# Kernel tuning notes

Measured on AMD Instinct MI355X. Metric: run time of the kernel, lower is better.

Reference implementation:

```python
import jax, jax.numpy as jnp
import numpy as np

B, S, D, H = 4, 2048, 1024, 16
DK = D // H


def setup_inputs() -> dict:
    key = jax.random.key(0)
    ks = jax.random.split(key, 12)
    def lin(k):
        # torch nn.Linear default init scale ~ 1/sqrt(fan_in); use small normal
        return jax.random.normal(k, (D, D), dtype=jnp.float32) * (1.0 / np.sqrt(D))
    inp = {
        "query": jax.random.normal(ks[0], (B, S, D), dtype=jnp.float32),
        "key":   jax.random.normal(ks[1], (B, S, D), dtype=jnp.float32),
        "value": jax.random.normal(ks[2], (B, S, D), dtype=jnp.float32),
        "Wq": lin(ks[3]), "bq": jax.random.normal(ks[4], (D,), dtype=jnp.float32) * 0.01,
        "Wk": lin(ks[5]), "bk": jax.random.normal(ks[6], (D,), dtype=jnp.float32) * 0.01,
        "Wv": lin(ks[7]), "bv": jax.random.normal(ks[8], (D,), dtype=jnp.float32) * 0.01,
        "Wo": lin(ks[9]), "bo": jax.random.normal(ks[10], (D,), dtype=jnp.float32) * 0.01,
        # causal mask, True = attend (masked_fill where mask == 0)
        "causal_mask": jnp.tril(jnp.ones((S, S), dtype=bool))[None, None, :, :],
    }
    return inp


def reference(query, key, value, Wq, bq, Wk, bk, Wv, bv, Wo, bo, causal_mask):
    # Linear projections (torch Linear: y = x @ W.T + b), split heads -> [B,H,S,DK]
    def proj(x, W, b):
        return (x @ W.T + b).reshape(B, S, H, DK).transpose(0, 2, 1, 3)
    Q = proj(query, Wq, bq)
    K = proj(key, Wk, bk)
    V = proj(value, Wv, bv)
    scale = 1.0 / jnp.sqrt(jnp.float32(DK))
    scores = jnp.einsum('bhqd,bhkd->bhqk', Q, K) * scale  # [B,H,S,S]
    scores = jnp.where(causal_mask, scores, -jnp.inf)
    attn = jax.nn.softmax(scores, axis=-1)
    out = jnp.einsum('bhqk,bhkd->bhqd', attn, V)  # [B,H,S,DK]
    out = out.transpose(0, 2, 1, 3).reshape(B, S, D)
    return out @ Wo.T + bo
```

## Files before the change

kernel.cpp:

```cpp
#include <hip/hip_runtime.h>
#include <stdint.h>

#define SLEN   2048
#define DMODEL 1024
#define NHEAD  16
#define DKH    64
#define BATCH  4

typedef unsigned short ushort_t;
typedef __bf16         bf16x8 __attribute__((ext_vector_type(8)));
typedef unsigned short u16x8  __attribute__((ext_vector_type(8)));
typedef unsigned short u16x4  __attribute__((ext_vector_type(4)));
typedef unsigned int   u32x4  __attribute__((ext_vector_type(4)));
typedef float          f32x4  __attribute__((ext_vector_type(4)));

#define QSCALE 0.18033688f

__device__ __forceinline__ ushort_t f2bf(float f) {
  unsigned int u = __builtin_bit_cast(unsigned int, f);
  u += 0x7fffu + ((u >> 16) & 1u);
  return (ushort_t)(u >> 16);
}
__device__ __forceinline__ unsigned pk2(float a, float b) {
  const unsigned ua = __builtin_bit_cast(unsigned, a) + 0x8000u;
  const unsigned ub = __builtin_bit_cast(unsigned, b) + 0x8000u;
  return __builtin_amdgcn_perm(ub, ua, 0x07060302u);
}
__device__ __forceinline__ u16x8 cvt8f(const float* p) {
  f32x4 a = *(const f32x4*)p;
  f32x4 b = *(const f32x4*)(p + 4);
  u32x4 w;
  w[0] = pk2(a[0], a[1]);
  w[1] = pk2(a[2], a[3]);
  w[2] = pk2(b[0], b[1]);
  w[3] = pk2(b[2], b[3]);
  return __builtin_bit_cast(u16x8, w);
}

typedef __attribute__((address_space(1))) void gvoid_t;
typedef __attribute__((address_space(3))) void lvoid_t;
__device__ __forceinline__ void gld_lds16(const void* g, void* l) {
  __builtin_amdgcn_global_load_lds((gvoid_t*)(g), (lvoid_t*)(l), 16, 0, 0);
}

__device__ __forceinline__ int swz(int row, int c) {
  return row * 64 + (c ^ ((row & 7) * 8));
}
__device__ __forceinline__ int sx4(int r) { return (r ^ (r >> 2)) & 3; }

__global__ __launch_bounds__(256) void cvt_all(
    const float* __restrict__ Wq, const float* __restrict__ Wk,
    const float* __restrict__ Wv, const float* __restrict__ Wo,
    const float* __restrict__ q, const float* __restrict__ k,
    const float* __restrict__ v,
    ushort_t* __restrict__ Wbf, ushort_t* __restrict__ Xq,
    ushort_t* __restrict__ Xk,  ushort_t* __restrict__ Xv) {
  const int b = blockIdx.x;
  if (b < 2048) {
    const int gid = b * 256 + threadIdx.x;
    const int seg = gid >> 17;
    const int off = (gid & 131071) * 8;
    const float* src = (seg == 0) ? Wq : (seg == 1) ? Wk : (seg == 2) ? Wv : Wo;
    *(u16x8*)&Wbf[((size_t)seg << 20) + off] = cvt8f(src + off);
  } else {
    const int gid = (b - 2048) * 256 + threadIdx.x;
    const int seg = gid >> 20;
    const size_t off = (size_t)(gid & 1048575) * 8;
    const float* src = (seg == 0) ? q : (seg == 1) ? k : v;
    ushort_t*    dst = (seg == 0) ? Xq : (seg == 1) ? Xk : Xv;
    *(u16x8*)&dst[off] = cvt8f(src + off);
  }
}

__device__ __forceinline__ void gemm_body(
    const ushort_t* __restrict__ X, const ushort_t* __restrict__ W,
    const float* __restrict__ bias, void* __restrict__ Outv, const int mode,
    const float sc)
{
  __shared__ ushort_t lA[3][256 * 32];
  __shared__ ushort_t lB[3][256 * 32];

  const int t    = threadIdx.x;
  const int lane = t & 63;
  const int w    = t >> 6;
  const int wr   = w >> 2;
  const int wc   = w & 3;
  const int m0   = blockIdx.x * 256;
  const int n0   = blockIdx.y * 256;
  const int col  = lane & 15;
  const int quad = lane >> 4;

  f32x4 acc[8][4];
#pragma unroll
  for (int i = 0; i < 8; i++)
#pragma unroll
    for (int j = 0; j < 4; j++) acc[i][j] = f32x4{0.f, 0.f, 0.f, 0.f};

  const int rS   = t >> 2;
  const int cS   = ((t & 3) ^ sx4(rS)) * 8;
  const ushort_t* gA0 = X + (size_t)(m0 + rS) * DMODEL + cS;
  const ushort_t* gA1 = gA0 + (size_t)128 * DMODEL;
  const ushort_t* gB0 = W + (size_t)(n0 + rS) * DMODEL + cS;
  const ushort_t* gB1 = gB0 + (size_t)128 * DMODEL;

#define STAGE_G(buf, k0) do {                        \
    gld_lds16(gA0 + (k0), &lA[buf][t * 8]);          \
    gld_lds16(gA1 + (k0), &lA[buf][t * 8 + 4096]);   \
    gld_lds16(gB0 + (k0), &lB[buf][t * 8]);          \
    gld_lds16(gB1 + (k0), &lB[buf][t * 8 + 4096]);   \
  } while (0)

  const int rchunk = (quad ^ ((col ^ (col >> 2)) & 3)) * 8;

  STAGE_G(0, 0);
  STAGE_G(1, 32);

  const int NT = DMODEL / 32;
  int cur = 0;
  for (int ks = 0; ks < NT; ++ks) {
    if (ks + 1 < NT) {
      asm volatile("s_waitcnt vmcnt(4)" ::: "memory");
    } else {
      asm volatile("s_waitcnt vmcnt(0)" ::: "memory");
    }
    __builtin_amdgcn_s_barrier();
    __builtin_amdgcn_sched_barrier(0);

    if (ks + 2 < NT) {
      const int nb = (cur == 0) ? 2 : cur - 1;
      STAGE_G(nb, (ks + 2) * 32);
    }

    const ushort_t* cA = &lA[cur][0];
    const ushort_t* cB = &lB[cur][0];
    bf16x8 af[8], bfr[4];
#pragma unroll
    for (int mi = 0; mi < 8; mi++)
      af[mi] = __builtin_bit_cast(bf16x8,
          *(const u16x8*)&cA[(wr * 128 + mi * 16 + col) * 32 + rchunk]);
#pragma unroll
    for (int ni = 0; ni < 4; ni++)
      bfr[ni] = __builtin_bit_cast(bf16x8,
          *(const u16x8*)&cB[(wc * 64 + ni * 16 + col) * 32 + rchunk]);

    __builtin_amdgcn_s_setprio(1);
#pragma unroll
    for (int mi = 0; mi < 8; mi++)
#pragma unroll
      for (int ni = 0; ni < 4; ni++)
        acc[mi][ni] = __builtin_amdgcn_mfma_f32_16x16x32_bf16(
            af[mi], bfr[ni], acc[mi][ni], 0, 0, 0);
    __builtin_amdgcn_s_setprio(0);

    cur = (cur == 2) ? 0 : cur + 1;
  }
#undef STAGE_G

  const int b_ = (m0 + wr * 128) >> 11;
#pragma unroll
  for (int ni = 0; ni < 4; ni++) {
    const int n  = n0 + wc * 64 + ni * 16 + col;
    const float bn = bias[n];
    const float bns = bn * sc;
    const int h  = n >> 6, dk = n & (DKH - 1);
#pragma unroll
    for (int mi = 0; mi < 8; mi++) {
      if (mode == 2) {
        const int s0 = ((m0 + wr * 128 + mi * 16 + quad * 4) & (SLEN - 1));
        u16x4 pk;
#pragma unroll
        for (int r = 0; r < 4; r++) pk[r] = f2bf(acc[mi][ni][r] + bn);
        *(u16x4*)&((ushort_t*)Outv)[(((size_t)(b_ * NHEAD + h)) * DKH + dk) * SLEN + s0] = pk;
      } else if (mode == 1) {
#pragma unroll
        for (int r = 0; r < 4; r++) {
          const int m = m0 + wr * 128 + mi * 16 + quad * 4 + r;
          const int s = m & (SLEN - 1);
          ((ushort_t*)Outv)[(((size_t)(b_ * NHEAD + h)) * SLEN + s) * DKH + dk] =
              f2bf(fmaf(acc[mi][ni][r], sc, bns));
        }
      } else {
#pragma unroll
        for (int r = 0; r < 4; r++) {
          const int m = m0 + wr * 128 + mi * 16 + quad * 4 + r;
          ((float*)Outv)[(size_t)m * DMODEL + n] = acc[mi][ni][r] + bn;
        }
      }
    }
  }
}

__global__ __launch_bounds__(512, 2) void gemm_qkv(
    const ushort_t* Xq, const ushort_t* Xk, const ushort_t* Xv,
    const ushort_t* Wbf,
    const float* bq, const float* bk, const float* bv,
    ushort_t* Qh, ushort_t* Kh, ushort_t* VhT) {
  const int z = blockIdx.z;
  const ushort_t* X = (z == 0) ? Xq : (z == 1) ? Xk : Xv;
  const ushort_t* W = Wbf + ((size_t)z << 20);
  const float* bias = (z == 0) ? bq : (z == 1) ? bk : bv;
  ushort_t* out     = (z == 0) ? Qh : (z == 1) ? Kh : VhT;
  gemm_body(X, W, bias, out, (z == 2) ? 2 : 1, (z == 0) ? QSCALE : 1.0f);
}

__global__ __launch_bounds__(512, 2) void gemm_out(
    const ushort_t* X, const ushort_t* Wobf, const float* bo, float* Out) {
  gemm_body(X, Wobf, bo, Out, 0, 1.0f);
}

__global__ __launch_bounds__(256, 4) void flash_attn(
    const ushort_t* __restrict__ Qh, const ushort_t* __restrict__ Kh,
    const ushort_t* __restrict__ VhT, ushort_t* __restrict__ Out)
{
  __shared__ ushort_t lK[2 * 64 * 64];
  __shared__ ushort_t lV[2 * 64 * 64];
  __shared__ ushort_t lP[4 * 16 * 64];

  const int t    = threadIdx.x;
  const int lane = t & 63;
  const int w    = t >> 6;
  const int col  = lane & 15;
  const int quad = lane >> 4;
  const int bh   = blockIdx.y;
  const int x    = blockIdx.x;
  const int ntA  = x + 1;
  const int ntB  = 32 - x;
  const int q0A  = x * 64;
  const int q0B  = (31 - x) * 64;

  const ushort_t* Qb = Qh  + (size_t)bh * SLEN * DKH;
  const ushort_t* Kb = Kh  + (size_t)bh * SLEN * DKH;
  const ushort_t* Vt = VhT + (size_t)bh * DKH * SLEN;

  bf16x8 qfA[2], qfB[2];
  {
    const int ra = q0A + w * 16 + col;
    const int rb = q0B + w * 16 + col;
    qfA[0] = __builtin_bit_cast(bf16x8, *(const u16x8*)&Qb[(size_t)ra * DKH + quad * 8]);
    qfA[1] = __builtin_bit_cast(bf16x8, *(const u16x8*)&Qb[(size_t)ra * DKH + 32 + quad * 8]);
    qfB[0] = __builtin_bit_cast(bf16x8, *(const u16x8*)&Qb[(size_t)rb * DKH + quad * 8]);
    qfB[1] = __builtin_bit_cast(bf16x8, *(const u16x8*)&Qb[(size_t)rb * DKH + 32 + quad * 8]);
  }

  f32x4 accA[4], accB[4], laccA, laccB;
#pragma unroll
  for (int n2 = 0; n2 < 4; n2++) {
    accA[n2] = f32x4{0.f, 0.f, 0.f, 0.f};
    accB[n2] = f32x4{0.f, 0.f, 0.f, 0.f};
  }
  laccA = f32x4{0.f, 0.f, 0.f, 0.f};
  laccB = f32x4{0.f, 0.f, 0.f, 0.f};

  u16x8 ones_u;
#pragma unroll
  for (int i = 0; i < 8; ++i) ones_u[i] = 0x3F80;
  const bf16x8 onesf = __builtin_bit_cast(bf16x8, ones_u);

  const int fA   = t * 8;
  const int rowA = fA >> 6;
  const int innA = fA & 63;
  const int cA   = innA ^ ((rowA & 7) * 8);
  const int rowB = rowA + 32;
  const int cB   = innA ^ ((rowB & 7) * 8);
  const ushort_t* gK0 = Kb + (size_t)rowA * DKH + cA;
  const ushort_t* gK1 = Kb + (size_t)rowB * DKH + cB;
  const ushort_t* gV0 = Vt + (size_t)rowA * SLEN + cA;
  const ushort_t* gV1 = Vt + (size_t)rowB * SLEN + cB;
  ushort_t* sK0 = &lK[fA];
  ushort_t* sK1 = &lK[fA + 2048];
  ushort_t* sV0 = &lV[fA];
  ushort_t* sV1 = &lV[fA + 2048];

  ushort_t* lPw = &lP[w * 1024];

  auto compute = [&](const bf16x8* qf, f32x4* acc_o, f32x4& lacc,
                     const int q0, const bool diag, const int kb,
                     const ushort_t* Kc, const ushort_t* Vc) {
    f32x4 sacc[4];
#pragma unroll
    for (int nt = 0; nt < 4; nt++) sacc[nt] = f32x4{0.f, 0.f, 0.f, 0.f};
#pragma unroll
    for (int ks = 0; ks < 2; ++ks) {
#pragma unroll
      for (int nt = 0; nt < 4; ++nt) {
        bf16x8 kf = __builtin_bit_cast(bf16x8,
            *(const u16x8*)&Kc[swz(nt * 16 + col, ks * 32 + quad * 8)]);
        sacc[nt] = __builtin_amdgcn_mfma_f32_16x16x32_bf16(qf[ks], kf, sacc[nt], 0, 0, 0);
      }
    }
#pragma unroll
    for (int r = 0; r < 4; r++) {
#pragma unroll
      for (int nt = 0; nt < 4; nt++) {
        float p = exp2f(sacc[nt][r]);
        if (diag) {
          const int kg = kb + nt * 16 + col;
          const int qg = q0 + w * 16 + quad * 4 + r;
          if (kg > qg) p = 0.f;
        }
        lPw[swz(quad * 4 + r, nt * 16 + col)] = f2bf(p);
      }
    }
    asm volatile("s_waitcnt lgkmcnt(0)" ::: "memory");
#pragma unroll
    for (int ks = 0; ks < 2; ++ks) {
      bf16x8 pf = __builtin_bit_cast(bf16x8,
          *(const u16x8*)&lPw[swz(col, ks * 32 + quad * 8)]);
      lacc = __builtin_amdgcn_mfma_f32_16x16x32_bf16(pf, onesf, lacc, 0, 0, 0);
#pragma unroll
      for (int n2 = 0; n2 < 4; ++n2) {
        bf16x8 vf = __builtin_bit_cast(bf16x8,
            *(const u16x8*)&Vc[swz(n2 * 16 + col, ks * 32 + quad * 8)]);
        acc_o[n2] = __builtin_amdgcn_mfma_f32_16x16x32_bf16(pf, vf, acc_o[n2], 0, 0, 0);
      }
    }
  };

  gld_lds16(gK0, sK0);
  gld_lds16(gK1, sK1);
  gld_lds16(gV0, sV0);
  gld_lds16(gV1, sV1);

  for (int it = 0; it < ntB; ++it) {
    const int cur = it & 1;
    const int kb  = it * 64;
    const ushort_t* Kc = &lK[cur * 4096];
    const ushort_t* Vc = &lV[cur * 4096];

    if (it + 1 < ntB) {
      const size_t kb1 = (size_t)(it + 1) * 64;
      const int nb = (cur ^ 1) * 4096;
      gld_lds16(gK0 + kb1 * DKH, sK0 + nb);
      gld_lds16(gK1 + kb1 * DKH, sK1 + nb);
      gld_lds16(gV0 + kb1,       sV0 + nb);
      gld_lds16(gV1 + kb1,       sV1 + nb);
      asm volatile("s_waitcnt vmcnt(4)" ::: "memory");
    } else {
      asm volatile("s_waitcnt vmcnt(0)" ::: "memory");
    }
    __builtin_amdgcn_s_barrier();

    compute(qfB, accB, laccB, q0B, it == ntB - 1, kb, Kc, Vc);
    if (it < ntA)
      compute(qfA, accA, laccA, q0A, it == ntA - 1, kb, Kc, Vc);

    __builtin_amdgcn_s_barrier();
  }

  const int b_ = bh >> 4;
  const int h  = bh & (NHEAD - 1);
#pragma unroll
  for (int side = 0; side < 2; ++side) {
    const f32x4* ao = side ? accA : accB;
    const f32x4& la = side ? laccA : laccB;
    const int q0 = side ? q0A : q0B;
#pragma unroll
    for (int r = 0; r < 4; r++) {
      const int qg = q0 + w * 16 + quad * 4 + r;
      const float inv = 1.f / la[r];
#pragma unroll
      for (int n2 = 0; n2 < 4; n2++) {
        const size_t oidx = ((size_t)b_ * SLEN + qg) * DMODEL + h * DKH + n2 * 16 + col;
        Out[oidx] = f2bf(ao[n2][r] * inv);
      }
    }
  }
}

extern "C" void kernel_launch(void* const* d_in, const int* in_sizes, int n_in,
                              void* d_out, int out_size, void* d_ws, size_t ws_size,
                              hipStream_t stream) {
  (void)in_sizes; (void)n_in; (void)out_size; (void)ws_size;
  const float* q  = (const float*)d_in[0];
  const float* k  = (const float*)d_in[1];
  const float* v  = (const float*)d_in[2];
  const float* Wq = (const float*)d_in[3];
  const float* bq = (const float*)d_in[4];
  const float* Wk = (const float*)d_in[5];
  const float* bk = (const float*)d_in[6];
  const float* Wv = (const float*)d_in[7];
  const float* bv = (const float*)d_in[8];
  const float* Wo = (const float*)d_in[9];
  const float* bo = (const float*)d_in[10];

  ushort_t* ws = (ushort_t*)d_ws;
  const size_t NELEM = (size_t)BATCH * SLEN * DMODEL;
  ushort_t* Wbf = ws;
  ushort_t* Qh  = ws + 4 * (1u << 20);
  ushort_t* Kh  = Qh + NELEM;
  ushort_t* Xq  = Kh + NELEM;
  ushort_t* Xk  = Xq + NELEM;
  ushort_t* Ao  = Xq;
  ushort_t* VhT = (ushort_t*)d_out;
  ushort_t* Xv  = (ushort_t*)d_out + NELEM;

  hipLaunchKernelGGL(cvt_all, dim3(2048 + 12288), dim3(256), 0, stream,
                     Wq, Wk, Wv, Wo, q, k, v, Wbf, Xq, Xk, Xv);
  hipLaunchKernelGGL(gemm_qkv, dim3(32, 4, 3), dim3(512), 0, stream,
                     Xq, Xk, Xv, Wbf, bq, bk, bv, Qh, Kh, VhT);
  hipLaunchKernelGGL(flash_attn, dim3(16, BATCH * NHEAD), dim3(256), 0, stream,
                     Qh, Kh, VhT, Ao);
  hipLaunchKernelGGL(gemm_out, dim3(32, 4), dim3(512), 0, stream,
                     Ao, Wbf + (3u << 20), bo, (float*)d_out);
}
```

Before: 395.5 us.

## Deepen GEMM LDS pipeline to four stages with split A/B loads and ping-pong phases

The projection GEMM moves from a 3-buffer to a 4-buffer LDS ring, prefetching three k-tiles ahead. The A and B global-to-LDS loads are split across two half-iterations, each followed by a barrier and an MFMA half-block, in a ping-pong schedule. It also swaps the LDS swizzle pattern and precomputes fragment addresses. The aim is to hide global-load latency and overlap LDS reads with MFMA work, at the cost of 64KB of LDS, which may lower occupancy, and extra barriers per iteration.

```diff
diff --git a/kernel.cpp b/kernel.cpp
--- a/kernel.cpp
+++ b/kernel.cpp
@@ -46,7 +46,6 @@
 __device__ __forceinline__ int swz(int row, int c) {
   return row * 64 + (c ^ ((row & 7) * 8));
 }
-__device__ __forceinline__ int sx4(int r) { return (r ^ (r >> 2)) & 3; }
 
 __global__ __launch_bounds__(256) void cvt_all(
     const float* __restrict__ Wq, const float* __restrict__ Wk,
@@ -77,8 +76,8 @@
     const float* __restrict__ bias, void* __restrict__ Outv, const int mode,
     const float sc)
 {
-  __shared__ ushort_t lA[3][256 * 32];
-  __shared__ ushort_t lB[3][256 * 32];
+  __shared__ ushort_t lA[4][8192];
+  __shared__ ushort_t lB[4][8192];
 
   const int t    = threadIdx.x;
   const int lane = t & 63;
@@ -96,65 +95,89 @@
 #pragma unroll
     for (int j = 0; j < 4; j++) acc[i][j] = f32x4{0.f, 0.f, 0.f, 0.f};
 
-  const int rS   = t >> 2;
-  const int cS   = ((t & 3) ^ sx4(rS)) * 8;
-  const ushort_t* gA0 = X + (size_t)(m0 + rS) * DMODEL + cS;
+  const int rS  = t >> 2;
+  const int csw = ((t & 3) ^ ((rS >> 1) & 3)) * 8;
+  const ushort_t* gA0 = X + (size_t)(m0 + rS) * DMODEL + csw;
   const ushort_t* gA1 = gA0 + (size_t)128 * DMODEL;
-  const ushort_t* gB0 = W + (size_t)(n0 + rS) * DMODEL + cS;
+  const ushort_t* gB0 = W + (size_t)(n0 + rS) * DMODEL + csw;
   const ushort_t* gB1 = gB0 + (size_t)128 * DMODEL;
 
-#define STAGE_G(buf, k0) do {                        \
-    gld_lds16(gA0 + (k0), &lA[buf][t * 8]);          \
-    gld_lds16(gA1 + (k0), &lA[buf][t * 8 + 4096]);   \
-    gld_lds16(gB0 + (k0), &lB[buf][t * 8]);          \
-    gld_lds16(gB1 + (k0), &lB[buf][t * 8 + 4096]);   \
+#define STAGE_A(buf, k0) do {                       \
+    gld_lds16(gA0 + (k0), &lA[buf][t * 8]);         \
+    gld_lds16(gA1 + (k0), &lA[buf][t * 8 + 4096]);  \
   } while (0)
-
-  const int rchunk = (quad ^ ((col ^ (col >> 2)) & 3)) * 8;
-
-  STAGE_G(0, 0);
-  STAGE_G(1, 32);
+#define STAGE_B(buf, k0) do {                       \
+    gld_lds16(gB0 + (k0), &lB[buf][t * 8]);         \
+    gld_lds16(gB1 + (k0), &lB[buf][t * 8 + 4096]);  \
+  } while (0)
+
+  int adrA[8], adrB[4];
+#pragma unroll
+  for (int mi = 0; mi < 8; mi++) {
+    const int r = wr * 128 + mi * 16 + col;
+    adrA[mi] = r * 32 + ((quad ^ ((r >> 1) & 3)) * 8);
+  }
+#pragma unroll
+  for (int ni = 0; ni < 4; ni++) {
+    const int r = wc * 64 + ni * 16 + col;
+    adrB[ni] = r * 32 + ((quad ^ ((r >> 1) & 3)) * 8);
+  }
+
+  STAGE_A(0, 0);  STAGE_B(0, 0);
+  STAGE_A(1, 32); STAGE_B(1, 32);
+  STAGE_A(2, 64); STAGE_B(2, 64);
 
   const int NT = DMODEL / 32;
-  int cur = 0;
   for (int ks = 0; ks < NT; ++ks) {
-    if (ks + 1 < NT) {
-      asm volatile("s_waitcnt vmcnt(4)" ::: "memory");
-    } else {
-      asm volatile("s_waitcnt vmcnt(0)" ::: "memory");
-    }
+    if (ks < NT - 2)       asm volatile("s_waitcnt vmcnt(8)" ::: "memory");
+    else if (ks == NT - 2) asm volatile("s_waitcnt vmcnt(4)" ::: "memory");
+    else                   asm volatile("s_waitcnt vmcnt(0)" ::: "memory");
     __builtin_amdgcn_s_barrier();
     __builtin_amdgcn_sched_barrier(0);
 
-    if (ks + 2 < NT) {
-      const int nb = (cur == 0) ? 2 : cur - 1;
-      STAGE_G(nb, (ks + 2) * 32);
-    }
-
-    const ushort_t* cA = &lA[cur][0];
-    const ushort_t* cB = &lB[cur][0];
+    const int s3 = (ks + 3) & 3;
+    const int k3 = (ks + 3) * 32;
+    const ushort_t* cA = &lA[ks & 3][0];
+    const ushort_t* cB = &lB[ks & 3][0];
+
+    if (ks + 3 < NT) STAGE_A(s3, k3);
     bf16x8 af[8], bfr[4];
 #pragma unroll
-    for (int mi = 0; mi < 8; mi++)
-      af[mi] = __builtin_bit_cast(bf16x8,
-          *(const u16x8*)&cA[(wr * 128 + mi * 16 + col) * 32 + rchunk]);
+    for (int mi = 0; mi < 4; mi++)
+      af[mi] = __builtin_bit_cast(bf16x8, *(const u16x8*)&cA[adrA[mi]]);
 #pragma unroll
     for (int ni = 0; ni < 4; ni++)
-      bfr[ni] = __builtin_bit_cast(bf16x8,
-          *(const u16x8*)&cB[(wc * 64 + ni * 16 + col) * 32 + rchunk]);
-
+      bfr[ni] = __builtin_bit_cast(bf16x8, *(const u16x8*)&cB[adrB[ni]]);
+    __builtin_amdgcn_s_barrier();
+    asm volatile("s_waitcnt lgkmcnt(0)" ::: "memory");
+    __builtin_amdgcn_sched_barrier(0);
     __builtin_amdgcn_s_setprio(1);
 #pragma unroll
-    for (int mi = 0; mi < 8; mi++)
+    for (int mi = 0; mi < 4; mi++)
 #pragma unroll
       for (int ni = 0; ni < 4; ni++)
         acc[mi][ni] = __builtin_amdgcn_mfma_f32_16x16x32_bf16(
             af[mi], bfr[ni], acc[mi][ni], 0, 0, 0);
     __builtin_amdgcn_s_setprio(0);
 
-    cur = (cur == 2) ? 0 : cur + 1;
-  }
-#undef STAGE_G
+    if (ks + 3 < NT) STAGE_B(s3, k3);
+#pragma unroll
+    for (int mi = 4; mi < 8; mi++)
+      af[mi] = __builtin_bit_cast(bf16x8, *(const u16x8*)&cA[adrA[mi]]);
+    __builtin_amdgcn_s_barrier();
+    asm volatile("s_waitcnt lgkmcnt(0)" ::: "memory");
+    __builtin_amdgcn_sched_barrier(0);
+    __builtin_amdgcn_s_setprio(1);
+#pragma unroll
+    for (int mi = 4; mi < 8; mi++)
+#pragma unroll
+      for (int ni = 0; ni < 4; ni++)
+        acc[mi][ni] = __builtin_amdgcn_mfma_f32_16x16x32_bf16(
+            af[mi], bfr[ni], acc[mi][ni], 0, 0, 0);
+    __builtin_amdgcn_s_setprio(0);
+  }
+#undef STAGE_A
+#undef STAGE_B
 
   const int b_ = (m0 + wr * 128) >> 11;
 #pragma unroll
```

New measurement: 407.4 us. 1.03x slower.
